# Optimization experiments

Hardware: AMD Instinct MI355X
Metric: run time of the kernel (lower is better)

## Reference

```python
import jax, jax.numpy as jnp
import numpy as np

NUM_EDGE = 5
NUM_CHANNELS = 2
NUM_NODES = 2048
W_IN = 256
W_OUT = 128
NUM_CLASS = 16
NUM_LAYERS = 2


def gtconv(A, w):
    """Softmax-weighted mix of edge-type adjacencies.
    A: [E, N, N], w: [E, C] -> [C, N, N].
    Equivalent to concatenating COO edge lists scaled by filter[j, i] and
    summing duplicates (what the scipy round-trip does implicitly)."""
    f = jax.nn.softmax(w, axis=0)  # softmax over edge types (dim=0)
    return jnp.einsum('enm,ec->cnm', A, f)


def degree_normalize(H):
    """GTN.normalization: deg = scatter_add over col, value *= deg[col]^-1 (col scaling).
    H: [C, N, N]; deg over rows (axis=1) gives per-column in-degree."""
    deg = H.sum(axis=1)  # [C, N]
    dinv = jnp.where(deg > 0, 1.0 / jnp.where(deg > 0, deg, 1.0), 0.0)
    return H * dinv[:, None, :]


def setup_inputs() -> dict:
    key = jax.random.key(0)
    ks = jax.random.split(key, 8)
    A = jax.random.uniform(ks[0], (NUM_EDGE, NUM_NODES, NUM_NODES), dtype=jnp.float32)
    h = jax.random.normal(ks[1], (NUM_NODES, W_IN), dtype=jnp.float32)
    # GTConv weights: init std=0.01 as in reset_parameters
    w1 = jax.random.normal(ks[2], (NUM_EDGE, NUM_CHANNELS), dtype=jnp.float32) * 0.01
    w2 = jax.random.normal(ks[3], (NUM_EDGE, NUM_CHANNELS), dtype=jnp.float32) * 0.01
    w_layers = jax.random.normal(ks[4], (NUM_LAYERS - 1, NUM_EDGE, NUM_CHANNELS), dtype=jnp.float32) * 0.01
    gcn_w = jax.random.normal(ks[5], (W_IN, W_OUT), dtype=jnp.float32) * (1.0 / np.sqrt(W_IN))
    gcn_b = jnp.zeros((W_OUT,), dtype=jnp.float32)
    lin1_w = jax.random.normal(ks[6], (W_OUT * NUM_CHANNELS, W_OUT), dtype=jnp.float32) * (1.0 / np.sqrt(W_OUT * NUM_CHANNELS))
    lin1_b = jnp.zeros((W_OUT,), dtype=jnp.float32)
    lin2_w = jax.random.normal(ks[7], (W_OUT, NUM_CLASS), dtype=jnp.float32) * (1.0 / np.sqrt(W_OUT))
    lin2_b = jnp.zeros((NUM_CLASS,), dtype=jnp.float32)
    return {"A": A, "h": h, "w1": w1, "w2": w2, "w_layers": w_layers,
            "gcn_w": gcn_w, "gcn_b": gcn_b, "lin1_w": lin1_w, "lin1_b": lin1_b,
            "lin2_w": lin2_w, "lin2_b": lin2_b}


def reference(A, h, w1, w2, w_layers, gcn_w, gcn_b, lin1_w, lin1_b, lin2_w, lin2_b):
    # Layer 0 (first=True): H[c] = conv1(A)[c] @ conv2(A)[c], then degree norm.
    H = jnp.einsum('cnk,ckm->cnm', gtconv(A, w1), gtconv(A, w2))
    H = degree_normalize(H)
    # Layers 1..L-1 (first=False): H[c] = H[c] @ conv(A)[c], then degree norm.
    for i in range(w_layers.shape[0]):
        B = gtconv(A, w_layers[i])
        H = jnp.einsum('cnk,ckm->cnm', H, B)
        H = degree_normalize(H)
    # Shared GCN per channel (DGL GraphConv, norm='both'): weight first (w_in > w_out),
    # src out-degree^-1/2 scaling, aggregate along edges src->dst, dst in-degree^-1/2.
    hw = h @ gcn_w                                   # [N, w_out]
    dout = jnp.clip(H.sum(axis=2), 1.0, None) ** -0.5  # [C, N] src norm
    din = jnp.clip(H.sum(axis=1), 1.0, None) ** -0.5   # [C, N] dst norm
    agg = jnp.einsum('cnm,cnd->cmd', H, dout[:, :, None] * hw[None])  # dst m gathers from src n
    X = jax.nn.relu(agg * din[:, :, None] + gcn_b)   # [C, N, w_out]
    # Concatenate channels along feature dim (channel-major, matching th.cat order)
    X = jnp.transpose(X, (1, 0, 2)).reshape(H.shape[1], -1)  # [N, C*w_out]
    X = jax.nn.relu(X @ lin1_w + lin1_b)
    return X @ lin2_w + lin2_b
```

## Files before the change

### kernel.cpp

```cpp
#include <hip/hip_runtime.h>

typedef unsigned short u16;
typedef __attribute__((ext_vector_type(4))) float f32x4;
typedef __attribute__((ext_vector_type(8))) __bf16 bf16x8;
typedef __attribute__((ext_vector_type(8))) unsigned short us8;

#define NN (2048ull*2048ull)

__device__ __forceinline__ u16 f2b(float x){
  union { float f; unsigned u; } v; v.f = x;
  unsigned r = v.u + 0x7FFFu + ((v.u >> 16) & 1u);
  return (u16)(r >> 16);
}
__device__ __forceinline__ float b2f(u16 x){
  union { unsigned u; float f; } v; v.u = ((unsigned)x) << 16; return v.f;
}

__global__ __launch_bounds__(256)
void k_zero(float4* __restrict__ p, int n4){
  const float4 z = {0.f,0.f,0.f,0.f};
  for (int i = blockIdx.x*256 + threadIdx.x; i < n4; i += gridDim.x*256)
    p[i] = z;
}

__global__ __launch_bounds__(256)
void k_mix(const float* __restrict__ A,
           const float* __restrict__ w1, const float* __restrict__ w2,
           const float* __restrict__ wl,
           u16* __restrict__ A1T, u16* __restrict__ A2T, u16* __restrict__ BT,
           float* __restrict__ sA1, float* __restrict__ deg2){
  __shared__ u16 lt[4][32][68];
  const int t = threadIdx.x;
  const int mg = t & 7, ng = t >> 3;
  const int m0 = blockIdx.x * 32, n0 = blockIdx.y * 64;
  float f[3][2][5];
  #pragma unroll
  for (int s=0;s<3;s++){
    const float* w = (s==0) ? w1 : (s==1) ? w2 : wl;
    #pragma unroll
    for (int c=0;c<2;c++){
      float m = -1e30f;
      #pragma unroll
      for (int e=0;e<5;e++) m = fmaxf(m, w[e*2+c]);
      float sum = 0.f;
      #pragma unroll
      for (int e=0;e<5;e++){ f[s][c][e] = __expf(w[e*2+c]-m); sum += f[s][c][e]; }
      float inv = 1.f/sum;
      #pragma unroll
      for (int e=0;e<5;e++) f[s][c][e] *= inv;
    }
  }

  ushort4 reg[6][2];
  #pragma unroll
  for (int rr=0; rr<2; ++rr){
    const int nl = ng*2 + rr;
    const size_t off = (size_t)(n0+nl)*2048 + m0 + mg*4;
    float4 a0 = *(const float4*)&A[off];
    float4 a1 = *(const float4*)&A[NN + off];
    float4 a2 = *(const float4*)&A[2*NN + off];
    float4 a3 = *(const float4*)&A[3*NN + off];
    float4 a4 = *(const float4*)&A[4*NN + off];
    float ax[4][5] = {{a0.x,a1.x,a2.x,a3.x,a4.x},
                      {a0.y,a1.y,a2.y,a3.y,a4.y},
                      {a0.z,a1.z,a2.z,a3.z,a4.z},
                      {a0.w,a1.w,a2.w,a3.w,a4.w}};
    #pragma unroll
    for (int c=0;c<2;c++){
      #pragma unroll
      for (int j=0;j<4;j++){
        float s1=0.f,s2=0.f,s3=0.f;
        #pragma unroll
        for (int e=0;e<5;e++){
          s1 += ax[j][e]*f[0][c][e];
          s2 += ax[j][e]*f[1][c][e];
          s3 += ax[j][e]*f[2][c][e];
        }
        ((u16*)&reg[0+c][rr])[j] = f2b(s1);
        ((u16*)&reg[2+c][rr])[j] = f2b(s2);
        ((u16*)&reg[4+c][rr])[j] = f2b(s3);
      }
    }
  }

  const int row = t >> 3, seg = t & 7;

  #pragma unroll
  for (int sc=0; sc<4; ++sc){
    #pragma unroll
    for (int j=0;j<4;j++){
      ushort2 o;
      o.x = ((const u16*)&reg[sc][0])[j];
      o.y = ((const u16*)&reg[sc][1])[j];
      *(ushort2*)&lt[sc][mg*4+j][ng*2] = o;
    }
  }
  __syncthreads();
  #pragma unroll
  for (int sc=0; sc<4; ++sc){
    u16* __restrict__ dst = (sc<2) ? A1T : A2T;
    const int c = sc & 1;
    us8 v0 = *(const us8*)&lt[sc][row][seg*8];
    u16* __restrict__ p = dst + (size_t)c*NN + (size_t)(m0+row)*2048 + n0 + seg*8;
    *(us8*)p = v0;
    if (sc < 2){
      float part = 0.f;
      #pragma unroll
      for (int q=0;q<8;q++) part += b2f(v0[q]);
      part += __shfl_xor(part, 1); part += __shfl_xor(part, 2);
      part += __shfl_xor(part, 4);
      if (seg == 0) atomicAdd(&sA1[c*2048 + m0 + row], part);
    }
  }
  __syncthreads();
  #pragma unroll
  for (int c=0;c<2;c++){
    #pragma unroll
    for (int j=0;j<4;j++){
      ushort2 o;
      o.x = ((const u16*)&reg[4+c][0])[j];
      o.y = ((const u16*)&reg[4+c][1])[j];
      *(ushort2*)&lt[c][mg*4+j][ng*2] = o;
    }
  }
  __syncthreads();
  #pragma unroll
  for (int c=0;c<2;c++){
    us8 v0 = *(const us8*)&lt[c][row][seg*8];
    u16* __restrict__ p = BT + (size_t)c*NN + (size_t)(m0+row)*2048 + n0 + seg*8;
    *(us8*)p = v0;
    float part = 0.f;
    #pragma unroll
    for (int q=0;q<8;q++) part += b2f(v0[q]);
    part += __shfl_xor(part, 1); part += __shfl_xor(part, 2);
    part += __shfl_xor(part, 4);
    if (seg == 0) atomicAdd(&deg2[c*2048 + m0 + row], part);
  }
}

__global__ __launch_bounds__(256)
void k_post1(const u16* __restrict__ A2T, const u16* __restrict__ BT,
             const float* __restrict__ sA1, const float* __restrict__ deg2,
             float* __restrict__ deg1, float* __restrict__ v1){
  const int b = blockIdx.x;
  const int t = threadIdx.x;
  if (b < 1024){
    const int g = b*4 + (t >> 6);
    const int lane = t & 63;
    const int c = g >> 11, j = g & 2047;
    const u16* __restrict__ row = A2T + (size_t)c*NN + (size_t)j*2048;
    const float* __restrict__ sv = sA1 + c*2048;
    float s = 0.f;
    #pragma unroll
    for (int it=0; it<4; ++it){
      const int k = it*512 + lane*8;
      us8 v = *(const us8*)&row[k];
      const float4 f0 = *(const float4*)&sv[k];
      const float4 f1 = *(const float4*)&sv[k+4];
      s += b2f(v[0])*f0.x + b2f(v[1])*f0.y + b2f(v[2])*f0.z + b2f(v[3])*f0.w
         + b2f(v[4])*f1.x + b2f(v[5])*f1.y + b2f(v[6])*f1.z + b2f(v[7])*f1.w;
    }
    s += __shfl_xor(s, 1);  s += __shfl_xor(s, 2);  s += __shfl_xor(s, 4);
    s += __shfl_xor(s, 8);  s += __shfl_xor(s, 16); s += __shfl_xor(s, 32);
    if (lane == 0) deg1[c*2048 + j] = s;
  } else {
    __shared__ float w[64];
    const int bx = b - 1024;
    const int x = bx & 7, y = (bx >> 3) & 31, c = bx >> 8;
    const int n = x * 256 + t;
    const int m0 = y * 64;
    if (t < 64){
      float d = deg2[c*2048 + m0 + t];
      w[t] = d > 0.f ? 1.f/d : 0.f;
    }
    __syncthreads();
    const u16* __restrict__ p = BT + (size_t)c*NN + (size_t)m0*2048 + n;
    float s = 0.f;
    #pragma unroll 4
    for (int m=0;m<64;m++)
      s += b2f(p[(size_t)m*2048]) * w[m];
    atomicAdd(&v1[c*2048 + n], s);
  }
}

template<int MODE>
__global__ __launch_bounds__(256)
void k_wsum(const u16* __restrict__ MT, const float* __restrict__ va,
            const float* __restrict__ vb, float* __restrict__ outv){
  __shared__ float w[64];
  const int t = threadIdx.x;
  const int n = blockIdx.x * 256 + t;
  const int m0 = blockIdx.y * 64;
  const int c = blockIdx.z;
  if (t < 64){
    const int m = c*2048 + m0 + t;
    float x;
    if (MODE == 1){ float d = va[m]; x = (d > 0.f ? 1.f/d : 0.f) * vb[m]; }
    else { x = va[m]; }
    w[t] = x;
  }
  __syncthreads();
  const u16* __restrict__ p = MT + (size_t)c*NN + (size_t)m0*2048 + n;
  float s = 0.f;
  #pragma unroll 4
  for (int m=0;m<64;m++)
    s += b2f(p[(size_t)m*2048]) * w[m];
  atomicAdd(&outv[c*2048 + n], s);
}

__global__ __launch_bounds__(256)
void k_hwpt(const float* __restrict__ h, const float* __restrict__ W,
            const float* __restrict__ rowsum, u16* __restrict__ PT){
  __shared__ float lh[8][256];
  int t = threadIdx.x;
  int n0 = blockIdx.x * 8;
  for (int idx = t; idx < 8*256; idx += 256)
    lh[idx >> 8][idx & 255] = h[(size_t)(n0 + (idx>>8))*256 + (idx&255)];
  __syncthreads();
  int d = t & 127, half = t >> 7;
  float acc[4];
  #pragma unroll
  for (int nn=0;nn<4;nn++) acc[nn] = 0.f;
  for (int k=0;k<256;k++){
    float wv = W[(size_t)k*128 + d];
    #pragma unroll
    for (int nn=0;nn<4;nn++) acc[nn] += lh[half*4+nn][k]*wv;
  }
  #pragma unroll
  for (int c=0;c<2;c++){
    ushort4 o;
    #pragma unroll
    for (int nn=0;nn<4;nn++){
      int n = n0 + half*4 + nn;
      float dv = rsqrtf(fmaxf(rowsum[c*2048 + n], 1.0f));
      ((u16*)&o)[nn] = f2b(dv * acc[nn]);
    }
    *(ushort4*)&PT[((size_t)c*128 + d)*2048 + n0 + half*4] = o;
  }
}

__global__ __launch_bounds__(256, 2)
void k_gemm3(const u16* __restrict__ A, const u16* __restrict__ Bt, float* __restrict__ Agg){
  __shared__ u16 lA[128*64];
  __shared__ u16 lB[128*64];
  const int tid = threadIdx.x;
  const int bm = blockIdx.x, bk = blockIdx.y, cc = blockIdx.z;
  const u16* __restrict__ Ab = A + (size_t)cc*NN + (size_t)(bm*128)*2048 + bk*256;
  const u16* __restrict__ Bb = Bt + (size_t)cc*(128*2048) + bk*256;
  float* __restrict__ Cb = Agg + (size_t)cc*2048*128 + (size_t)(bm*128)*128;
  const int wid = tid >> 6, lane = tid & 63;
  const int wr = wid >> 1, wc = wid & 1;
  const int fl = lane & 15, fk = (lane >> 4) << 3;
  const int srow = (wid << 3) + (lane >> 3);
  const int scol = (lane & 7) << 3;

  f32x4 acc[4][4];
  const f32x4 zero = {0.f,0.f,0.f,0.f};
  #pragma unroll
  for (int i=0;i<4;i++)
    #pragma unroll
    for (int jj=0;jj<4;jj++) acc[i][jj] = zero;

  for (int k0 = 0; k0 < 256; k0 += 64){
    #pragma unroll
    for (int it = 0; it < 4; ++it){
      int r = it*32 + srow;
      __builtin_amdgcn_global_load_lds(
        (const __attribute__((address_space(1))) void*)(Ab + (size_t)r*2048 + k0 + scol),
        (__attribute__((address_space(3))) void*)(&lA[(it*32 + (wid<<3))*64]), 16, 0, 0);
      __builtin_amdgcn_global_load_lds(
        (const __attribute__((address_space(1))) void*)(Bb + (size_t)r*2048 + k0 + scol),
        (__attribute__((address_space(3))) void*)(&lB[(it*32 + (wid<<3))*64]), 16, 0, 0);
    }
    __syncthreads();
    #pragma unroll
    for (int ks = 0; ks < 2; ++ks){
      bf16x8 af[4], bfr[4];
      #pragma unroll
      for (int mi=0;mi<4;mi++)
        af[mi] = *reinterpret_cast<const bf16x8*>(&lA[(wr*64 + mi*16 + fl)*64 + ks*32 + fk]);
      #pragma unroll
      for (int ni=0;ni<4;ni++)
        bfr[ni] = *reinterpret_cast<const bf16x8*>(&lB[(wc*64 + ni*16 + fl)*64 + ks*32 + fk]);
      #pragma unroll
      for (int mi=0;mi<4;mi++)
        #pragma unroll
        for (int ni=0;ni<4;ni++)
          acc[mi][ni] = __builtin_amdgcn_mfma_f32_16x16x32_bf16(af[mi], bfr[ni], acc[mi][ni], 0, 0, 0);
    }
    __syncthreads();
  }
  const int rbase = (lane >> 4) << 2;
  #pragma unroll
  for (int mi=0;mi<4;mi++)
    #pragma unroll
    for (int ni=0;ni<4;ni++)
      #pragma unroll
      for (int r=0;r<4;r++)
        atomicAdd(&Cb[(size_t)(wr*64 + mi*16 + rbase + r)*128 + wc*64 + ni*16 + fl],
                  acc[mi][ni][r]);
}

template<bool SCALE>
__global__ __launch_bounds__(256)
void k_qt(const float* __restrict__ Agg, const float* __restrict__ deg1,
          u16* __restrict__ QT){
  __shared__ u16 lq[128][36];
  const int t = threadIdx.x;
  const int m0 = blockIdx.x * 32, c = blockIdx.y;
  const int d4 = (t & 31) * 4, mr = t >> 5;
  #pragma unroll
  for (int p4=0; p4<4; ++p4){
    const int m = m0 + p4*8 + mr;
    float4 s = *(const float4*)&Agg[((size_t)c*2048 + m)*128 + d4];
    if (SCALE){
      float dg = deg1[c*2048 + m];
      float di = dg > 0.f ? 1.f/dg : 0.f;
      s.x *= di; s.y *= di; s.z *= di; s.w *= di;
    }
    const int ml = p4*8 + mr;
    lq[d4+0][ml] = f2b(s.x); lq[d4+1][ml] = f2b(s.y);
    lq[d4+2][ml] = f2b(s.z); lq[d4+3][ml] = f2b(s.w);
  }
  __syncthreads();
  const int d = t >> 1, half = t & 1;
  u16* __restrict__ dst = QT + ((size_t)c*128 + d)*2048 + m0 + half*16;
  #pragma unroll
  for (int q=0;q<4;q++){
    ushort4 o;
    o.x = lq[d][half*16 + q*4 + 0];
    o.y = lq[d][half*16 + q*4 + 1];
    o.z = lq[d][half*16 + q*4 + 2];
    o.w = lq[d][half*16 + q*4 + 3];
    *(ushort4*)&dst[q*4] = o;
  }
}

__global__ __launch_bounds__(256)
void k_head(const float* __restrict__ agg3, const float* __restrict__ deg2,
            const float* __restrict__ gb,
            const float* __restrict__ W1, const float* __restrict__ b1,
            const float* __restrict__ W2, const float* __restrict__ b2,
            float* __restrict__ out){
  __shared__ float lx[8][256];
  __shared__ float lt[8][132];
  int t = threadIdx.x;
  int n0 = blockIdx.x * 8;
  for (int idx = t; idx < 512; idx += 256){
    int row = idx >> 6;
    int q = idx & 63;
    int c = q >> 5, d4 = (q & 31) * 4;
    float dg = deg2[c*2048 + n0 + row];
    float di = dg > 0.f ? 1.f/dg : 0.f;
    float4 s = *(const float4*)&agg3[((size_t)c*2048 + n0 + row)*128 + d4];
    const float4 bv = *(const float4*)&gb[d4];
    s.x = fmaxf(s.x*di + bv.x, 0.f); s.y = fmaxf(s.y*di + bv.y, 0.f);
    s.z = fmaxf(s.z*di + bv.z, 0.f); s.w = fmaxf(s.w*di + bv.w, 0.f);
    *(float4*)&lx[row][c*128 + d4] = s;
  }
  __syncthreads();
  int d = t & 127, half = t >> 7;
  float acc[4];
  #pragma unroll
  for (int nn=0;nn<4;nn++) acc[nn] = 0.f;
  for (int k=0;k<256;k++){
    float wv = W1[(size_t)k*128 + d];
    #pragma unroll
    for (int nn=0;nn<4;nn++) acc[nn] += lx[half*4+nn][k]*wv;
  }
  float bb = b1[d];
  #pragma unroll
  for (int nn=0;nn<4;nn++){
    float v = acc[nn] + bb;
    lt[half*4+nn][d] = v > 0.f ? v : 0.f;
  }
  __syncthreads();
  if (t < 128){
    int row = t >> 4, q = t & 15;
    float s = b2[q];
    for (int dd=0; dd<128; dd++) s += lt[row][dd] * W2[(size_t)dd*16 + q];
    out[(size_t)(n0+row)*16 + q] = s;
  }
}

extern "C" void kernel_launch(void* const* d_in, const int* in_sizes, int n_in,
                              void* d_out, int out_size, void* d_ws, size_t ws_size,
                              hipStream_t stream){
  const float* A   = (const float*)d_in[0];
  const float* h   = (const float*)d_in[1];
  const float* w1  = (const float*)d_in[2];
  const float* w2  = (const float*)d_in[3];
  const float* wl  = (const float*)d_in[4];
  const float* gw  = (const float*)d_in[5];
  const float* gb  = (const float*)d_in[6];
  const float* l1w = (const float*)d_in[7];
  const float* l1b = (const float*)d_in[8];
  const float* l2w = (const float*)d_in[9];
  const float* l2b = (const float*)d_in[10];
  float* out = (float*)d_out;
  char* ws = (char*)d_ws;

  const size_t SZ = 2*NN*2;
  const size_t AGG = (size_t)2*2048*128*4;
  u16*  A1T  = (u16*)(ws);
  u16*  A2T  = (u16*)(ws + 1*SZ);
  u16*  BT   = (u16*)(ws + 2*SZ);
  char* tail = ws + 3*SZ;
  u16*  PT     = (u16*)tail;
  u16*  Q1T    = (u16*)(tail + 1048576);
  u16*  Q2T    = (u16*)(tail + 2*1048576);
  float* sA1   = (float*)(tail + 3*1048576);
  float* deg1  = sA1 + 4096;
  float* deg2  = deg1 + 4096;
  float* v1    = deg2 + 4096;
  float* v3    = v1 + 4096;
  float* rowsum= v3 + 4096;
  float* agg1  = rowsum + 4096;
  float* agg2  = agg1 + 2*2048*128;
  float* agg3  = agg2 + 2*2048*128;
  const size_t ZBYTES = 6*4096*4 + 3*AGG;

  const size_t TOTAL = 3*SZ + 3*1048576 + ZBYTES;
  if (ws_size < TOTAL){ hipMemsetAsync(d_out, 0, (size_t)out_size*4, stream); return; }

  k_zero<<<1024, 256, 0, stream>>>((float4*)sA1, (int)(ZBYTES/16));

  k_mix<<<dim3(64,32), 256, 0, stream>>>(A, w1, w2, wl, A1T, A2T, BT, sA1, deg2);
  k_post1<<<1536, 256, 0, stream>>>(A2T, BT, sA1, deg2, deg1, v1);
  k_wsum<1><<<dim3(8,32,2), 256, 0, stream>>>(A2T, deg1, v1, v3);
  k_wsum<2><<<dim3(8,32,2), 256, 0, stream>>>(A1T, v3, v3, rowsum);
  k_hwpt<<<256, 256, 0, stream>>>(h, gw, rowsum, PT);
  k_gemm3<<<dim3(16,8,2), 256, 0, stream>>>(A1T, PT, agg1);
  k_qt<false><<<dim3(64,2), 256, 0, stream>>>(agg1, deg1, Q1T);
  k_gemm3<<<dim3(16,8,2), 256, 0, stream>>>(A2T, Q1T, agg2);
  k_qt<true><<<dim3(64,2), 256, 0, stream>>>(agg2, deg1, Q2T);
  k_gemm3<<<dim3(16,8,2), 256, 0, stream>>>(BT, Q2T, agg3);
  k_head<<<256, 256, 0, stream>>>(agg3, deg2, gb, l1w, l1b, l2w, l2b, out);
}
```

Before: 153.3 us.

## Store intermediate bf16 matrices in contiguous 32x64 tile-blocked layout

Result: faster. 149.1 us (-2.8%).

```diff
diff --git a/kernel.cpp b/kernel.cpp
--- a/kernel.cpp
+++ b/kernel.cpp
@@ -6,6 +6,7 @@
 typedef __attribute__((ext_vector_type(8))) unsigned short us8;
 
 #define NN (2048ull*2048ull)
+
 
 __device__ __forceinline__ u16 f2b(float x){
   union { float f; unsigned u; } v; v.f = x;
@@ -84,6 +85,7 @@
   }
 
   const int row = t >> 3, seg = t & 7;
+  const size_t tb = (((size_t)blockIdx.y*64 + blockIdx.x) << 11) + (size_t)t*8;
 
   #pragma unroll
   for (int sc=0; sc<4; ++sc){
@@ -101,8 +103,7 @@
     u16* __restrict__ dst = (sc<2) ? A1T : A2T;
     const int c = sc & 1;
     us8 v0 = *(const us8*)&lt[sc][row][seg*8];
-    u16* __restrict__ p = dst + (size_t)c*NN + (size_t)(m0+row)*2048 + n0 + seg*8;
-    *(us8*)p = v0;
+    *(us8*)&dst[(size_t)c*NN + tb] = v0;
     if (sc < 2){
       float part = 0.f;
       #pragma unroll
@@ -127,8 +128,7 @@
   #pragma unroll
   for (int c=0;c<2;c++){
     us8 v0 = *(const us8*)&lt[c][row][seg*8];
-    u16* __restrict__ p = BT + (size_t)c*NN + (size_t)(m0+row)*2048 + n0 + seg*8;
-    *(us8*)p = v0;
+    *(us8*)&BT[(size_t)c*NN + tb] = v0;
     float part = 0.f;
     #pragma unroll
     for (int q=0;q<8;q++) part += b2f(v0[q]);
@@ -148,13 +148,15 @@
     const int g = b*4 + (t >> 6);
     const int lane = t & 63;
     const int c = g >> 11, j = g & 2047;
-    const u16* __restrict__ row = A2T + (size_t)c*NN + (size_t)j*2048;
+    const u16* __restrict__ base = A2T + (size_t)c*NN
+        + ((size_t)(j>>5) << 11) + (size_t)((j&31) << 6)
+        + ((size_t)(lane>>3) << 17) + (size_t)(lane&7)*8;
     const float* __restrict__ sv = sA1 + c*2048;
     float s = 0.f;
     #pragma unroll
     for (int it=0; it<4; ++it){
       const int k = it*512 + lane*8;
-      us8 v = *(const us8*)&row[k];
+      us8 v = *(const us8*)&base[(size_t)it << 20];
       const float4 f0 = *(const float4*)&sv[k];
       const float4 f1 = *(const float4*)&sv[k+4];
       s += b2f(v[0])*f0.x + b2f(v[1])*f0.y + b2f(v[2])*f0.z + b2f(v[3])*f0.w
@@ -174,11 +176,15 @@
       w[t] = d > 0.f ? 1.f/d : 0.f;
     }
     __syncthreads();
-    const u16* __restrict__ p = BT + (size_t)c*NN + (size_t)m0*2048 + n;
+    const u16* __restrict__ base = BT + (size_t)c*NN
+        + ((size_t)((n>>6)*64 + (m0>>5)) << 11) + (n & 63);
     float s = 0.f;
     #pragma unroll 4
-    for (int m=0;m<64;m++)
-      s += b2f(p[(size_t)m*2048]) * w[m];
+    for (int m=0;m<32;m++)
+      s += b2f(base[m*64]) * w[m];
+    #pragma unroll 4
+    for (int m=0;m<32;m++)
+      s += b2f(base[2048 + m*64]) * w[32+m];
     atomicAdd(&v1[c*2048 + n], s);
   }
 }
@@ -200,11 +206,15 @@
     w[t] = x;
   }
   __syncthreads();
-  const u16* __restrict__ p = MT + (size_t)c*NN + (size_t)m0*2048 + n;
+  const u16* __restrict__ base = MT + (size_t)c*NN
+      + ((size_t)((n>>6)*64 + (m0>>5)) << 11) + (n & 63);
   float s = 0.f;
   #pragma unroll 4
-  for (int m=0;m<64;m++)
-    s += b2f(p[(size_t)m*2048]) * w[m];
+  for (int m=0;m<32;m++)
+    s += b2f(base[m*64]) * w[m];
+  #pragma unroll 4
+  for (int m=0;m<32;m++)
+    s += b2f(base[2048 + m*64]) * w[32+m];
   atomicAdd(&outv[c*2048 + n], s);
 }
 
@@ -245,7 +255,6 @@
   __shared__ u16 lB[128*64];
   const int tid = threadIdx.x;
   const int bm = blockIdx.x, bk = blockIdx.y, cc = blockIdx.z;
-  const u16* __restrict__ Ab = A + (size_t)cc*NN + (size_t)(bm*128)*2048 + bk*256;
   const u16* __restrict__ Bb = Bt + (size_t)cc*(128*2048) + bk*256;
   float* __restrict__ Cb = Agg + (size_t)cc*2048*128 + (size_t)(bm*128)*128;
   const int wid = tid >> 6, lane = tid & 63;
@@ -264,10 +273,13 @@
   for (int k0 = 0; k0 < 256; k0 += 64){
     #pragma unroll
     for (int it = 0; it < 4; ++it){
+      const u16* srcA = A + (size_t)cc*NN
+          + (((size_t)((bk*4 + (k0>>6))*64 + bm*4 + it)) << 11)
+          + (srow << 6) + scol;
+      __builtin_amdgcn_global_load_lds(
+        (const __attribute__((address_space(1))) void*)srcA,
+        (__attribute__((address_space(3))) void*)(&lA[(it*32 + (wid<<3))*64]), 16, 0, 0);
       int r = it*32 + srow;
-      __builtin_amdgcn_global_load_lds(
-        (const __attribute__((address_space(1))) void*)(Ab + (size_t)r*2048 + k0 + scol),
-        (__attribute__((address_space(3))) void*)(&lA[(it*32 + (wid<<3))*64]), 16, 0, 0);
       __builtin_amdgcn_global_load_lds(
         (const __attribute__((address_space(1))) void*)(Bb + (size_t)r*2048 + k0 + scol),
         (__attribute__((address_space(3))) void*)(&lB[(it*32 + (wid<<3))*64]), 16, 0, 0);
```
